# Kernel tuning notes

Hardware: AMD Instinct MI355X
Metric: run time of the kernel (lower is better)

Reference implementation:

```python
import jax, jax.numpy as jnp
import numpy as np

N_NODES = 50000
N_EDGES = 600000
D_IN, D_H1, D_H2 = 128, 128, 64


def setup_inputs() -> dict:
    key = jax.random.key(0)
    ks = jax.random.split(key, 8)
    x = jax.random.normal(ks[0], (N_NODES, D_IN), dtype=jnp.float32)
    edge_index = jax.random.randint(ks[1], (2, N_EDGES), 0, N_NODES, dtype=jnp.int64)
    # Glorot-style init for GCN weights, uniform for biases
    W1 = jax.random.normal(ks[2], (D_IN, D_H1), dtype=jnp.float32) / np.sqrt(D_IN)
    b1 = jnp.zeros((D_H1,), dtype=jnp.float32)
    W2 = jax.random.normal(ks[3], (D_H1, D_H2), dtype=jnp.float32) / np.sqrt(D_H1)
    b2 = jnp.zeros((D_H2,), dtype=jnp.float32)
    W3 = jax.random.normal(ks[4], (D_H2, 1), dtype=jnp.float32) / np.sqrt(D_H2)
    b3 = jnp.zeros((1,), dtype=jnp.float32)
    return {"x": x, "edge_index": edge_index, "W1": W1, "b1": b1,
            "W2": W2, "b2": b2, "W3": W3, "b3": b3}


def _gcn_norm(edge_index, n_nodes, dtype):
    # Add self-loops, then symmetric normalization deg^-1/2 * deg^-1/2 (PyG gcn_norm).
    loop = jnp.arange(n_nodes, dtype=edge_index.dtype)
    src = jnp.concatenate([edge_index[0], loop])
    dst = jnp.concatenate([edge_index[1], loop])
    deg = jax.ops.segment_sum(jnp.ones_like(dst, dtype=dtype), dst, num_segments=n_nodes)
    dinv = jnp.where(deg > 0, jax.lax.rsqrt(deg), 0.0)
    norm = dinv[src] * dinv[dst]  # [E+N]
    return src, dst, norm


def _gcn_conv(x, src, dst, norm, W, b, n_nodes):
    h = x @ W                       # [N, F_out]
    msg = h[src] * norm[:, None]    # gather + scale: [E+N, F_out]
    out = jax.ops.segment_sum(msg, dst, num_segments=n_nodes)  # scatter-add
    return out + b


def reference(x, edge_index, W1, b1, W2, b2, W3, b3):
    n = x.shape[0]
    src, dst, norm = _gcn_norm(edge_index, n, x.dtype)
    h = jax.nn.relu(_gcn_conv(x, src, dst, norm, W1, b1, n))
    # dropout is identity in eval mode
    h = jax.nn.relu(_gcn_conv(h, src, dst, norm, W2, b2, n))
    return h @ W3 + b3  # [N, 1]
```

## Files before the change

### kernel.cpp

```cpp
#include <hip/hip_runtime.h>

#define N_NODES 50000
#define N_EDGES 600000
#define CAP 64
#define GB1 ((N_NODES + 63) / 64)
#define FB  ((N_EDGES + 255) / 256)

typedef unsigned int u32;
typedef unsigned short u16;
typedef __attribute__((ext_vector_type(8))) short short8;
typedef __attribute__((ext_vector_type(4))) float f32x4;

__device__ __forceinline__ u16 f2bf(float f) {
    u32 u = __float_as_uint(f);
    u32 r = (u + 0x7fffu + ((u >> 16) & 1u)) >> 16;
    return (u16)r;
}
__device__ __forceinline__ float bf_lo(u32 u) { return __uint_as_float(u << 16); }
__device__ __forceinline__ float bf_hi(u32 u) { return __uint_as_float(u & 0xffff0000u); }


__global__ __launch_bounds__(256) void fill_transpose(const int* __restrict__ ei,
                                                      int* __restrict__ deg,
                                                      int* __restrict__ col,
                                                      const float* __restrict__ W1,
                                                      const float* __restrict__ W2,
                                                      u16* __restrict__ W1t,
                                                      u16* __restrict__ W2t) {
    int b = blockIdx.x, t = threadIdx.x;
    if (b < FB) {
        int e = b * 256 + t;
        if (e < N_EDGES) {
            int s = ei[e];
            int d = ei[N_EDGES + e];
            int r = atomicAdd(&deg[d], 1);
            if (r < CAP) col[((size_t)d << 6) + r] = s;
        }
    } else if (b < FB + 64) {
        int i = (b - FB) * 256 + t;
        int n = i >> 7, k = i & 127;
        W1t[i] = f2bf(W1[k * 128 + n]);
    } else {
        int j = (b - FB - 64) * 256 + t;
        int n = j >> 7, k = j & 127;
        W2t[j] = f2bf(W2[k * 64 + n]);
    }
}


#define SL 136

__global__ __launch_bounds__(256) void gemm1_k(const float* __restrict__ A,
                                               const u16* __restrict__ Bt,
                                               u16* __restrict__ out) {
    __shared__ u16 As[64 * SL];
    __shared__ u16 Bs[128 * SL];
    const int tid = threadIdx.x;
    const int m0 = blockIdx.x * 64;
    {
        int row = tid >> 2, c0 = (tid & 3) * 32;
        bool ok = (m0 + row) < N_NODES;
        const float4* src = (const float4*)&A[(size_t)(m0 + row) * 128 + c0];
        u16* dst = &As[row * SL + c0];
#pragma unroll
        for (int i = 0; i < 8; ++i) {
            float4 v = ok ? src[i] : make_float4(0.f, 0.f, 0.f, 0.f);
            u32 lo = (u32)f2bf(v.x) | ((u32)f2bf(v.y) << 16);
            u32 hi = (u32)f2bf(v.z) | ((u32)f2bf(v.w) << 16);
            *(uint2*)&dst[i * 4] = make_uint2(lo, hi);
        }
    }
    {
        int n = tid >> 1, h = (tid & 1) * 64;
        const uint4* src = (const uint4*)&Bt[n * 128 + h];
        u16* dst = &Bs[n * SL + h];
#pragma unroll
        for (int i = 0; i < 8; ++i) *(uint4*)&dst[i * 8] = src[i];
    }
    __syncthreads();

    const int l = tid & 63, w = tid >> 6;
    const int q = l >> 4, r16 = l & 15;
    const int m_off = w * 16;
    f32x4 acc[8] = {};
#pragma unroll
    for (int kt = 0; kt < 128; kt += 32) {
        short8 a = *(const short8*)&As[(m_off + r16) * SL + kt + q * 8];
        short8 bb[8];
#pragma unroll
        for (int tn = 0; tn < 8; ++tn)
            bb[tn] = *(const short8*)&Bs[(tn * 16 + r16) * SL + kt + q * 8];
#pragma unroll
        for (int tn = 0; tn < 8; ++tn)
            acc[tn] = __builtin_amdgcn_mfma_f32_16x16x32_bf16(a, bb[tn], acc[tn], 0, 0, 0);
    }
#pragma unroll
    for (int r = 0; r < 4; ++r) {
        int row = m0 + m_off + q * 4 + r;
        if (row < N_NODES) {
#pragma unroll
            for (int tn = 0; tn < 8; ++tn)
                out[(size_t)row * 128 + tn * 16 + r16] = f2bf(acc[tn][r]);
        }
    }
}


__global__ __launch_bounds__(256) void agg_gemm2(const u16* __restrict__ hs,
                                                 const int* __restrict__ deg,
                                                 const int* __restrict__ col,
                                                 const float* __restrict__ bias,
                                                 const u16* __restrict__ Bt,
                                                 u16* __restrict__ out) {
    __shared__ u16 As[64 * SL];
    __shared__ u16 Bs[64 * SL];
    const int tid = threadIdx.x;
    const int m0 = blockIdx.x * 64;
    {
        int n = tid >> 2, s0 = (tid & 3) * 32;
        const uint4* src = (const uint4*)&Bt[n * 128 + s0];
        u16* dst = &Bs[n * SL + s0];
#pragma unroll
        for (int i = 0; i < 4; ++i) *(uint4*)&dst[i * 8] = src[i];
    }
    const uint4* rows = (const uint4*)hs;
    const int lane = tid & 15;
    const int sub = lane & 7;
    const int fo = lane * 8;
#pragma unroll
    for (int p = 0; p < 4; ++p) {
        int nl = p * 16 + (tid >> 4);
        int node = m0 + nl;
        uint4 pk = make_uint4(0, 0, 0, 0);
        if (node < N_NODES) {
            int dg = deg[node];
            float dv = rsqrtf((float)(dg + 1));
            float acc[8];
            uint4 sv = rows[(size_t)node * 16 + lane];
            acc[0] = dv * bf_lo(sv.x); acc[1] = dv * bf_hi(sv.x);
            acc[2] = dv * bf_lo(sv.y); acc[3] = dv * bf_hi(sv.y);
            acc[4] = dv * bf_lo(sv.z); acc[5] = dv * bf_hi(sv.z);
            acc[6] = dv * bf_lo(sv.w); acc[7] = dv * bf_hi(sv.w);
            const int* crow = col + ((size_t)node << 6);
            int c = crow[sub];
            c = (sub < dg) ? c : 0;
            float scr = rsqrtf((float)(deg[c] + 1));
            float sc = (sub < dg) ? scr : 0.f;
            for (int r0 = 0; r0 < dg; r0 += 8) {
                int jn = r0 + 8 + sub;
                int cn = crow[jn & (CAP - 1)];
                cn = (jn < dg) ? cn : 0;
                float scnr = rsqrtf((float)(deg[cn] + 1));
                float scn = (jn < dg) ? scnr : 0.f;
#pragma unroll
                for (int jj = 0; jj < 8; ++jj) {
                    int cj = __shfl(c, jj, 16);
                    float scj = __shfl(sc, jj, 16);
                    uint4 v = rows[(size_t)cj * 16 + lane];
                    acc[0] = fmaf(scj, bf_lo(v.x), acc[0]);
                    acc[1] = fmaf(scj, bf_hi(v.x), acc[1]);
                    acc[2] = fmaf(scj, bf_lo(v.y), acc[2]);
                    acc[3] = fmaf(scj, bf_hi(v.y), acc[3]);
                    acc[4] = fmaf(scj, bf_lo(v.z), acc[4]);
                    acc[5] = fmaf(scj, bf_hi(v.z), acc[5]);
                    acc[6] = fmaf(scj, bf_lo(v.w), acc[6]);
                    acc[7] = fmaf(scj, bf_hi(v.w), acc[7]);
                }
                c = cn; sc = scn;
            }
            u32 w0[4];
#pragma unroll
            for (int jq = 0; jq < 4; ++jq) {
                u16 a = f2bf(fmaxf(fmaf(dv, acc[2 * jq], bias[fo + 2 * jq]), 0.f));
                u16 bq = f2bf(fmaxf(fmaf(dv, acc[2 * jq + 1], bias[fo + 2 * jq + 1]), 0.f));
                w0[jq] = (u32)a | ((u32)bq << 16);
            }
            pk = make_uint4(w0[0], w0[1], w0[2], w0[3]);
        }
        *(uint4*)&As[nl * SL + fo] = pk;
    }
    __syncthreads();

    const int l = tid & 63, w = tid >> 6;
    const int q = l >> 4, r16 = l & 15;
    const int m_off = w * 16;
    f32x4 acc2[4] = {};
#pragma unroll
    for (int kt = 0; kt < 128; kt += 32) {
        short8 a = *(const short8*)&As[(m_off + r16) * SL + kt + q * 8];
        short8 bb[4];
#pragma unroll
        for (int tn = 0; tn < 4; ++tn)
            bb[tn] = *(const short8*)&Bs[(tn * 16 + r16) * SL + kt + q * 8];
#pragma unroll
        for (int tn = 0; tn < 4; ++tn)
            acc2[tn] = __builtin_amdgcn_mfma_f32_16x16x32_bf16(a, bb[tn], acc2[tn], 0, 0, 0);
    }
#pragma unroll
    for (int r = 0; r < 4; ++r) {
        int row = m0 + m_off + q * 4 + r;
        if (row < N_NODES) {
            float dvr = rsqrtf((float)(deg[row] + 1));
#pragma unroll
            for (int tn = 0; tn < 4; ++tn)
                out[(size_t)row * 64 + tn * 16 + r16] = f2bf(acc2[tn][r] * dvr);
        }
    }
}


__global__ __launch_bounds__(256) void agg_final_bf(const u16* __restrict__ hs,
                                                    const int* __restrict__ deg,
                                                    const int* __restrict__ col,
                                                    const float* __restrict__ b2,
                                                    const float* __restrict__ W3,
                                                    const float* __restrict__ b3,
                                                    float* __restrict__ out) {
    int node = blockIdx.x * 32 + (threadIdx.x >> 3);
    int lane = threadIdx.x & 7;
    if (node >= N_NODES) return;
    const uint4* rows = (const uint4*)hs;
    int dg = deg[node];
    float acc[8] = {};
    auto accum = [&](uint4 v) {
        acc[0] += bf_lo(v.x); acc[1] += bf_hi(v.x);
        acc[2] += bf_lo(v.y); acc[3] += bf_hi(v.y);
        acc[4] += bf_lo(v.z); acc[5] += bf_hi(v.z);
        acc[6] += bf_lo(v.w); acc[7] += bf_hi(v.w);
    };
    accum(rows[(size_t)node * 8 + lane]);
    const int* crow = col + ((size_t)node << 6);
    int c = crow[lane];
    c = (lane < dg) ? c : 0;
    for (int r0 = 0; r0 < dg; r0 += 8) {
        int jn = r0 + 8 + lane;
        int cn = crow[jn & (CAP - 1)];
        cn = (jn < dg) ? cn : 0;
#pragma unroll
        for (int jj = 0; jj < 8; ++jj) {
            int cj = __shfl(c, jj, 8);
            uint4 v = rows[(size_t)cj * 8 + lane];
            uint4 vv = (r0 + jj < dg) ? v : make_uint4(0, 0, 0, 0);
            accum(vv);
        }
        c = cn;
    }
    float dv = rsqrtf((float)(dg + 1));
    int fo = lane * 8;
    float vsum = 0.f;
#pragma unroll
    for (int jq = 0; jq < 8; ++jq)
        vsum += fmaxf(fmaf(dv, acc[jq], b2[fo + jq]), 0.f) * W3[fo + jq];
#pragma unroll
    for (int m = 4; m > 0; m >>= 1) vsum += __shfl_xor(vsum, m, 64);
    if (lane == 0) out[node] = vsum + b3[0];
}


extern "C" void kernel_launch(void* const* d_in, const int* in_sizes, int n_in,
                              void* d_out, int out_size, void* d_ws, size_t ws_size,
                              hipStream_t stream) {
    const float* x  = (const float*)d_in[0];
    const int*   ei = (const int*)d_in[1];
    const float* W1 = (const float*)d_in[2];
    const float* b1 = (const float*)d_in[3];
    const float* W2 = (const float*)d_in[4];
    const float* b2 = (const float*)d_in[5];
    const float* W3 = (const float*)d_in[6];
    const float* b3 = (const float*)d_in[7];
    float* out = (float*)d_out;

    char* ws = (char*)d_ws;
    size_t off = 0;
    auto alloc = [&](size_t bytes) -> void* {
        void* p = ws + off;
        off = (off + bytes + 255) & ~(size_t)255;
        return p;
    };
    int* deg = (int*)alloc(N_NODES * sizeof(int));
    int* col = (int*)alloc(((size_t)N_NODES * CAP + 64) * sizeof(int));
    u16* W1t = (u16*)alloc(128 * 128 * sizeof(u16));
    u16* W2t = (u16*)alloc(64 * 128 * sizeof(u16));
    u16* hs1 = (u16*)alloc((size_t)N_NODES * 128 * sizeof(u16));
    u16* hs2 = (u16*)alloc((size_t)N_NODES * 64 * sizeof(u16));

    hipMemsetAsync(deg, 0, N_NODES * sizeof(int), stream);
    fill_transpose<<<FB + 96, 256, 0, stream>>>(ei, deg, col, W1, W2, W1t, W2t);
    gemm1_k<<<GB1, 256, 0, stream>>>(x, W1t, hs1);
    agg_gemm2<<<(N_NODES + 63) / 64, 256, 0, stream>>>(hs1, deg, col, b1, W2t, hs2);
    agg_final_bf<<<(N_NODES + 31) / 32, 256, 0, stream>>>(hs2, deg, col, b2, W3, b3, out);
}
```

Before: 168.1 us.

## Fuse all GCN stages into one persistent cooperative kernel with grid syncs

Replaces the memset and four separate kernel launches with a single cooperative persistent kernel. Grid-wide syncs separate the stages: zeroing and weight transposes, then the edge fill overlapped with gemm1, then aggregation plus gemm2, then the final aggregation. This removes launch gaps and lets the CSR fill and the first GEMM share one phase. The cost is a grid size capped by occupancy, which the largest LDS footprint (sized for gemm1) now sets for every phase, plus the expense of each grid barrier.

```diff
diff --git a/kernel.cpp b/kernel.cpp
--- a/kernel.cpp
+++ b/kernel.cpp
@@ -1,10 +1,15 @@
 #include <hip/hip_runtime.h>
+#include <hip/hip_cooperative_groups.h>
+
+namespace cg = cooperative_groups;
 
 #define N_NODES 50000
 #define N_EDGES 600000
 #define CAP 64
 #define GB1 ((N_NODES + 63) / 64)
 #define FB  ((N_EDGES + 255) / 256)
+#define AFB ((N_NODES + 31) / 32)
+#define SL 136
 
 typedef unsigned int u32;
 typedef unsigned short u16;
@@ -20,240 +25,236 @@
 __device__ __forceinline__ float bf_hi(u32 u) { return __uint_as_float(u & 0xffff0000u); }
 
 
-__global__ __launch_bounds__(256) void fill_transpose(const int* __restrict__ ei,
-                                                      int* __restrict__ deg,
-                                                      int* __restrict__ col,
-                                                      const float* __restrict__ W1,
-                                                      const float* __restrict__ W2,
-                                                      u16* __restrict__ W1t,
-                                                      u16* __restrict__ W2t) {
-    int b = blockIdx.x, t = threadIdx.x;
-    if (b < FB) {
-        int e = b * 256 + t;
-        if (e < N_EDGES) {
-            int s = ei[e];
-            int d = ei[N_EDGES + e];
-            int r = atomicAdd(&deg[d], 1);
-            if (r < CAP) col[((size_t)d << 6) + r] = s;
-        }
-    } else if (b < FB + 64) {
-        int i = (b - FB) * 256 + t;
+__global__ __launch_bounds__(256) void fused_k(
+    const float* __restrict__ x, const int* __restrict__ ei,
+    const float* __restrict__ W1, const float* __restrict__ b1,
+    const float* __restrict__ W2, const float* __restrict__ b2,
+    const float* __restrict__ W3, const float* __restrict__ b3,
+    float* __restrict__ out,
+    int* __restrict__ deg, int* __restrict__ col,
+    u16* __restrict__ W1t, u16* __restrict__ W2t,
+    u16* __restrict__ hs1, u16* __restrict__ hs2)
+{
+    __shared__ u16 As[64 * SL];
+    __shared__ u16 Bs[128 * SL];
+    cg::grid_group gg = cg::this_grid();
+    const int tid = threadIdx.x;
+    const int gsz = gridDim.x;
+    const int gtid = blockIdx.x * 256 + tid;
+    const int gstride = gsz * 256;
+
+    for (int i = gtid; i < N_NODES / 4; i += gstride)
+        ((int4*)deg)[i] = make_int4(0, 0, 0, 0);
+    for (int i = gtid; i < 128 * 128; i += gstride) {
         int n = i >> 7, k = i & 127;
         W1t[i] = f2bf(W1[k * 128 + n]);
-    } else {
-        int j = (b - FB - 64) * 256 + t;
-        int n = j >> 7, k = j & 127;
-        W2t[j] = f2bf(W2[k * 64 + n]);
-    }
-}
-
-
-#define SL 136
-
-__global__ __launch_bounds__(256) void gemm1_k(const float* __restrict__ A,
-                                               const u16* __restrict__ Bt,
-                                               u16* __restrict__ out) {
-    __shared__ u16 As[64 * SL];
-    __shared__ u16 Bs[128 * SL];
-    const int tid = threadIdx.x;
-    const int m0 = blockIdx.x * 64;
-    {
-        int row = tid >> 2, c0 = (tid & 3) * 32;
-        bool ok = (m0 + row) < N_NODES;
-        const float4* src = (const float4*)&A[(size_t)(m0 + row) * 128 + c0];
-        u16* dst = &As[row * SL + c0];
-#pragma unroll
-        for (int i = 0; i < 8; ++i) {
-            float4 v = ok ? src[i] : make_float4(0.f, 0.f, 0.f, 0.f);
-            u32 lo = (u32)f2bf(v.x) | ((u32)f2bf(v.y) << 16);
-            u32 hi = (u32)f2bf(v.z) | ((u32)f2bf(v.w) << 16);
-            *(uint2*)&dst[i * 4] = make_uint2(lo, hi);
-        }
-    }
-    {
-        int n = tid >> 1, h = (tid & 1) * 64;
-        const uint4* src = (const uint4*)&Bt[n * 128 + h];
-        u16* dst = &Bs[n * SL + h];
-#pragma unroll
-        for (int i = 0; i < 8; ++i) *(uint4*)&dst[i * 8] = src[i];
-    }
-    __syncthreads();
-
-    const int l = tid & 63, w = tid >> 6;
-    const int q = l >> 4, r16 = l & 15;
-    const int m_off = w * 16;
-    f32x4 acc[8] = {};
-#pragma unroll
-    for (int kt = 0; kt < 128; kt += 32) {
-        short8 a = *(const short8*)&As[(m_off + r16) * SL + kt + q * 8];
-        short8 bb[8];
-#pragma unroll
-        for (int tn = 0; tn < 8; ++tn)
-            bb[tn] = *(const short8*)&Bs[(tn * 16 + r16) * SL + kt + q * 8];
-#pragma unroll
-        for (int tn = 0; tn < 8; ++tn)
-            acc[tn] = __builtin_amdgcn_mfma_f32_16x16x32_bf16(a, bb[tn], acc[tn], 0, 0, 0);
-    }
-#pragma unroll
-    for (int r = 0; r < 4; ++r) {
-        int row = m0 + m_off + q * 4 + r;
-        if (row < N_NODES) {
+    }
+    for (int i = gtid; i < 64 * 128; i += gstride) {
+        int n = i >> 7, k = i & 127;
+        W2t[i] = f2bf(W2[k * 64 + n]);
+    }
+    __threadfence();
+    gg.sync();
+
+    for (int item = blockIdx.x; item < GB1 + FB; item += gsz) {
+        if (item >= GB1) {
+            int e = (item - GB1) * 256 + tid;
+            if (e < N_EDGES) {
+                int s = ei[e];
+                int d = ei[N_EDGES + e];
+                int r = atomicAdd(&deg[d], 1);
+                if (r < CAP) col[((size_t)d << 6) + r] = s;
+            }
+            continue;
+        }
+        const int m0 = item * 64;
+        __syncthreads();
+        {
+            int row = tid >> 2, c0 = (tid & 3) * 32;
+            bool ok = (m0 + row) < N_NODES;
+            const float4* src = (const float4*)&x[(size_t)(m0 + row) * 128 + c0];
+            u16* dst = &As[row * SL + c0];
+#pragma unroll
+            for (int i = 0; i < 8; ++i) {
+                float4 v = ok ? src[i] : make_float4(0.f, 0.f, 0.f, 0.f);
+                u32 lo = (u32)f2bf(v.x) | ((u32)f2bf(v.y) << 16);
+                u32 hi = (u32)f2bf(v.z) | ((u32)f2bf(v.w) << 16);
+                *(uint2*)&dst[i * 4] = make_uint2(lo, hi);
+            }
+        }
+        {
+            int n = tid >> 1, h = (tid & 1) * 64;
+            const uint4* src = (const uint4*)&W1t[n * 128 + h];
+            u16* dst = &Bs[n * SL + h];
+#pragma unroll
+            for (int i = 0; i < 8; ++i) *(uint4*)&dst[i * 8] = src[i];
+        }
+        __syncthreads();
+        const int l = tid & 63, w = tid >> 6;
+        const int q = l >> 4, r16 = l & 15;
+        const int m_off = w * 16;
+        f32x4 acc[8] = {};
+#pragma unroll
+        for (int kt = 0; kt < 128; kt += 32) {
+            short8 a = *(const short8*)&As[(m_off + r16) * SL + kt + q * 8];
+            short8 bb[8];
 #pragma unroll
             for (int tn = 0; tn < 8; ++tn)
-                out[(size_t)row * 128 + tn * 16 + r16] = f2bf(acc[tn][r]);
-        }
-    }
-}
-
-
-__global__ __launch_bounds__(256) void agg_gemm2(const u16* __restrict__ hs,
-                                                 const int* __restrict__ deg,
-                                                 const int* __restrict__ col,
-                                                 const float* __restrict__ bias,
-                                                 const u16* __restrict__ Bt,
-                                                 u16* __restrict__ out) {
-    __shared__ u16 As[64 * SL];
-    __shared__ u16 Bs[64 * SL];
-    const int tid = threadIdx.x;
-    const int m0 = blockIdx.x * 64;
-    {
-        int n = tid >> 2, s0 = (tid & 3) * 32;
-        const uint4* src = (const uint4*)&Bt[n * 128 + s0];
-        u16* dst = &Bs[n * SL + s0];
-#pragma unroll
-        for (int i = 0; i < 4; ++i) *(uint4*)&dst[i * 8] = src[i];
-    }
-    const uint4* rows = (const uint4*)hs;
-    const int lane = tid & 15;
-    const int sub = lane & 7;
-    const int fo = lane * 8;
-#pragma unroll
-    for (int p = 0; p < 4; ++p) {
-        int nl = p * 16 + (tid >> 4);
-        int node = m0 + nl;
-        uint4 pk = make_uint4(0, 0, 0, 0);
+                bb[tn] = *(const short8*)&Bs[(tn * 16 + r16) * SL + kt + q * 8];
+#pragma unroll
+            for (int tn = 0; tn < 8; ++tn)
+                acc[tn] = __builtin_amdgcn_mfma_f32_16x16x32_bf16(a, bb[tn], acc[tn], 0, 0, 0);
+        }
+#pragma unroll
+        for (int r = 0; r < 4; ++r) {
+            int row = m0 + m_off + q * 4 + r;
+            if (row < N_NODES) {
+#pragma unroll
+                for (int tn = 0; tn < 8; ++tn)
+                    hs1[(size_t)row * 128 + tn * 16 + r16] = f2bf(acc[tn][r]);
+            }
+        }
+    }
+    __threadfence();
+    gg.sync();
+
+    for (int item = blockIdx.x; item < GB1; item += gsz) {
+        const int m0 = item * 64;
+        __syncthreads();
+        {
+            int n = tid >> 2, s0 = (tid & 3) * 32;
+            const uint4* src = (const uint4*)&W2t[n * 128 + s0];
+            u16* dst = &Bs[n * SL + s0];
+#pragma unroll
+            for (int i = 0; i < 4; ++i) *(uint4*)&dst[i * 8] = src[i];
+        }
+        const uint4* rows = (const uint4*)hs1;
+        const int lane = tid & 15;
+        const int sub = lane & 7;
+        const int fo = lane * 8;
+#pragma unroll
+        for (int p = 0; p < 4; ++p) {
+            int nl = p * 16 + (tid >> 4);
+            int node = m0 + nl;
+            uint4 pk = make_uint4(0, 0, 0, 0);
+            if (node < N_NODES) {
+                int dg = deg[node];
+                float dv = rsqrtf((float)(dg + 1));
+                float acc[8];
+                uint4 sv = rows[(size_t)node * 16 + lane];
+                acc[0] = dv * bf_lo(sv.x); acc[1] = dv * bf_hi(sv.x);
+                acc[2] = dv * bf_lo(sv.y); acc[3] = dv * bf_hi(sv.y);
+                acc[4] = dv * bf_lo(sv.z); acc[5] = dv * bf_hi(sv.z);
+                acc[6] = dv * bf_lo(sv.w); acc[7] = dv * bf_hi(sv.w);
+                const int* crow = col + ((size_t)node << 6);
+                int c = crow[sub];
+                c = (sub < dg) ? c : 0;
+                float scr = rsqrtf((float)(deg[c] + 1));
+                float sc = (sub < dg) ? scr : 0.f;
+                for (int r0 = 0; r0 < dg; r0 += 8) {
+                    int jn = r0 + 8 + sub;
+                    int cn = crow[jn & (CAP - 1)];
+                    cn = (jn < dg) ? cn : 0;
+                    float scnr = rsqrtf((float)(deg[cn] + 1));
+                    float scn = (jn < dg) ? scnr : 0.f;
+#pragma unroll
+                    for (int jj = 0; jj < 8; ++jj) {
+                        int cj = __shfl(c, jj, 16);
+                        float scj = __shfl(sc, jj, 16);
+                        uint4 v = rows[(size_t)cj * 16 + lane];
+                        acc[0] = fmaf(scj, bf_lo(v.x), acc[0]);
+                        acc[1] = fmaf(scj, bf_hi(v.x), acc[1]);
+                        acc[2] = fmaf(scj, bf_lo(v.y), acc[2]);
+                        acc[3] = fmaf(scj, bf_hi(v.y), acc[3]);
+                        acc[4] = fmaf(scj, bf_lo(v.z), acc[4]);
+                        acc[5] = fmaf(scj, bf_hi(v.z), acc[5]);
+                        acc[6] = fmaf(scj, bf_lo(v.w), acc[6]);
+                        acc[7] = fmaf(scj, bf_hi(v.w), acc[7]);
+                    }
+                    c = cn; sc = scn;
+                }
+                u32 w0[4];
+#pragma unroll
+                for (int jq = 0; jq < 4; ++jq) {
+                    u16 a = f2bf(fmaxf(fmaf(dv, acc[2 * jq], b1[fo + 2 * jq]), 0.f));
+                    u16 bq = f2bf(fmaxf(fmaf(dv, acc[2 * jq + 1], b1[fo + 2 * jq + 1]), 0.f));
+                    w0[jq] = (u32)a | ((u32)bq << 16);
+                }
+                pk = make_uint4(w0[0], w0[1], w0[2], w0[3]);
+            }
+            *(uint4*)&As[nl * SL + fo] = pk;
+        }
+        __syncthreads();
+        const int l = tid & 63, w = tid >> 6;
+        const int q = l >> 4, r16 = l & 15;
+        const int m_off = w * 16;
+        f32x4 acc2[4] = {};
+#pragma unroll
+        for (int kt = 0; kt < 128; kt += 32) {
+            short8 a = *(const short8*)&As[(m_off + r16) * SL + kt + q * 8];
+            short8 bb[4];
+#pragma unroll
+            for (int tn = 0; tn < 4; ++tn)
+                bb[tn] = *(const short8*)&Bs[(tn * 16 + r16) * SL + kt + q * 8];
+#pragma unroll
+            for (int tn = 0; tn < 4; ++tn)
+                acc2[tn] = __builtin_amdgcn_mfma_f32_16x16x32_bf16(a, bb[tn], acc2[tn], 0, 0, 0);
+        }
+#pragma unroll
+        for (int r = 0; r < 4; ++r) {
+            int row = m0 + m_off + q * 4 + r;
+            if (row < N_NODES) {
+                float dvr = rsqrtf((float)(deg[row] + 1));
+#pragma unroll
+                for (int tn = 0; tn < 4; ++tn)
+                    hs2[(size_t)row * 64 + tn * 16 + r16] = f2bf(acc2[tn][r] * dvr);
+            }
+        }
+    }
+    __threadfence();
+    gg.sync();
+
+    for (int item = blockIdx.x; item < AFB; item += gsz) {
+        int node = item * 32 + (tid >> 3);
+        int lane = tid & 7;
         if (node < N_NODES) {
+            const uint4* rows = (const uint4*)hs2;
             int dg = deg[node];
-            float dv = rsqrtf((float)(dg + 1));
-            float acc[8];
-            uint4 sv = rows[(size_t)node * 16 + lane];
-            acc[0] = dv * bf_lo(sv.x); acc[1] = dv * bf_hi(sv.x);
-            acc[2] = dv * bf_lo(sv.y); acc[3] = dv * bf_hi(sv.y);
-            acc[4] = dv * bf_lo(sv.z); acc[5] = dv * bf_hi(sv.z);
-            acc[6] = dv * bf_lo(sv.w); acc[7] = dv * bf_hi(sv.w);
+            float acc[8] = {};
+            auto accum = [&](uint4 v) {
+                acc[0] += bf_lo(v.x); acc[1] += bf_hi(v.x);
+                acc[2] += bf_lo(v.y); acc[3] += bf_hi(v.y);
+                acc[4] += bf_lo(v.z); acc[5] += bf_hi(v.z);
+                acc[6] += bf_lo(v.w); acc[7] += bf_hi(v.w);
+            };
+            accum(rows[(size_t)node * 8 + lane]);
             const int* crow = col + ((size_t)node << 6);
-            int c = crow[sub];
-            c = (sub < dg) ? c : 0;
-            float scr = rsqrtf((float)(deg[c] + 1));
-            float sc = (sub < dg) ? scr : 0.f;
+            int c = crow[lane];
+            c = (lane < dg) ? c : 0;
             for (int r0 = 0; r0 < dg; r0 += 8) {
-                int jn = r0 + 8 + sub;
+                int jn = r0 + 8 + lane;
                 int cn = crow[jn & (CAP - 1)];
                 cn = (jn < dg) ? cn : 0;
-                float scnr = rsqrtf((float)(deg[cn] + 1));
-                float scn = (jn < dg) ? scnr : 0.f;
 #pragma unroll
                 for (int jj = 0; jj < 8; ++jj) {
-                    int cj = __shfl(c, jj, 16);
-                    float scj = __shfl(sc, jj, 16);
-                    uint4 v = rows[(size_t)cj * 16 + lane];
-                    acc[0] = fmaf(scj, bf_lo(v.x), acc[0]);
-                    acc[1] = fmaf(scj, bf_hi(v.x), acc[1]);
-                    acc[2] = fmaf(scj, bf_lo(v.y), acc[2]);
-                    acc[3] = fmaf(scj, bf_hi(v.y), acc[3]);
-                    acc[4] = fmaf(scj, bf_lo(v.z), acc[4]);
-                    acc[5] = fmaf(scj, bf_hi(v.z), acc[5]);
-                    acc[6] = fmaf(scj, bf_lo(v.w), acc[6]);
-                    acc[7] = fmaf(scj, bf_hi(v.w), acc[7]);
+                    int cj = __shfl(c, jj, 8);
+                    uint4 v = rows[(size_t)cj * 8 + lane];
+                    uint4 vv = (r0 + jj < dg) ? v : make_uint4(0, 0, 0, 0);
+                    accum(vv);
                 }
-                c = cn; sc = scn;
-            }
-            u32 w0[4];
-#pragma unroll
-            for (int jq = 0; jq < 4; ++jq) {
-                u16 a = f2bf(fmaxf(fmaf(dv, acc[2 * jq], bias[fo + 2 * jq]), 0.f));
-                u16 bq = f2bf(fmaxf(fmaf(dv, acc[2 * jq + 1], bias[fo + 2 * jq + 1]), 0.f));
-                w0[jq] = (u32)a | ((u32)bq << 16);
-            }
-            pk = make_uint4(w0[0], w0[1], w0[2], w0[3]);
-        }
-        *(uint4*)&As[nl * SL + fo] = pk;
-    }
-    __syncthreads();
-
-    const int l = tid & 63, w = tid >> 6;
-    const int q = l >> 4, r16 = l & 15;
-    const int m_off = w * 16;
-    f32x4 acc2[4] = {};
-#pragma unroll
-    for (int kt = 0; kt < 128; kt += 32) {
-        short8 a = *(const short8*)&As[(m_off + r16) * SL + kt + q * 8];
-        short8 bb[4];
-#pragma unroll
-        for (int tn = 0; tn < 4; ++tn)
-            bb[tn] = *(const short8*)&Bs[(tn * 16 + r16) * SL + kt + q * 8];
-#pragma unroll
-        for (int tn = 0; tn < 4; ++tn)
-            acc2[tn] = __builtin_amdgcn_mfma_f32_16x16x32_bf16(a, bb[tn], acc2[tn], 0, 0, 0);
-    }
-#pragma unroll
-    for (int r = 0; r < 4; ++r) {
-        int row = m0 + m_off + q * 4 + r;
-        if (row < N_NODES) {
-            float dvr = rsqrtf((float)(deg[row] + 1));
-#pragma unroll
-            for (int tn = 0; tn < 4; ++tn)
-                out[(size_t)row * 64 + tn * 16 + r16] = f2bf(acc2[tn][r] * dvr);
-        }
-    }
-}
-
-
-__global__ __launch_bounds__(256) void agg_final_bf(const u16* __restrict__ hs,
-                                                    const int* __restrict__ deg,
-                                                    const int* __restrict__ col,
-                                                    const float* __restrict__ b2,
-                                                    const float* __restrict__ W3,
-                                                    const float* __restrict__ b3,
-                                                    float* __restrict__ out) {
-    int node = blockIdx.x * 32 + (threadIdx.x >> 3);
-    int lane = threadIdx.x & 7;
-    if (node >= N_NODES) return;
-    const uint4* rows = (const uint4*)hs;
-    int dg = deg[node];
-    float acc[8] = {};
-    auto accum = [&](uint4 v) {
-        acc[0] += bf_lo(v.x); acc[1] += bf_hi(v.x);
-        acc[2] += bf_lo(v.y); acc[3] += bf_hi(v.y);
-        acc[4] += bf_lo(v.z); acc[5] += bf_hi(v.z);
-        acc[6] += bf_lo(v.w); acc[7] += bf_hi(v.w);
-    };
-    accum(rows[(size_t)node * 8 + lane]);
-    const int* crow = col + ((size_t)node << 6);
-    int c = crow[lane];
-    c = (lane < dg) ? c : 0;
-    for (int r0 = 0; r0 < dg; r0 += 8) {
-        int jn = r0 + 8 + lane;
-        int cn = crow[jn & (CAP - 1)];
-        cn = (jn < dg) ? cn : 0;
-#pragma unroll
-        for (int jj = 0; jj < 8; ++jj) {
-            int cj = __shfl(c, jj, 8);
-            uint4 v = rows[(size_t)cj * 8 + lane];
-            uint4 vv = (r0 + jj < dg) ? v : make_uint4(0, 0, 0, 0);
-            accum(vv);
-        }
-        c = cn;
-    }
-    float dv = rsqrtf((float)(dg + 1));
-    int fo = lane * 8;
-    float vsum = 0.f;
-#pragma unroll
-    for (int jq = 0; jq < 8; ++jq)
-        vsum += fmaxf(fmaf(dv, acc[jq], b2[fo + jq]), 0.f) * W3[fo + jq];
-#pragma unroll
-    for (int m = 4; m > 0; m >>= 1) vsum += __shfl_xor(vsum, m, 64);
-    if (lane == 0) out[node] = vsum + b3[0];
+                c = cn;
+            }
+            float dv = rsqrtf((float)(dg + 1));
+            int fo = lane * 8;
+            float vsum = 0.f;
+#pragma unroll
+            for (int jq = 0; jq < 8; ++jq)
+                vsum += fmaxf(fmaf(dv, acc[jq], b2[fo + jq]), 0.f) * W3[fo + jq];
+#pragma unroll
+            for (int m = 4; m > 0; m >>= 1) vsum += __shfl_xor(vsum, m, 64);
+            if (lane == 0) out[node] = vsum + b3[0];
+        }
+    }
 }
 
 
@@ -284,9 +285,21 @@
     u16* hs1 = (u16*)alloc((size_t)N_NODES * 128 * sizeof(u16));
     u16* hs2 = (u16*)alloc((size_t)N_NODES * 64 * sizeof(u16));
 
-    hipMemsetAsync(deg, 0, N_NODES * sizeof(int), stream);
-    fill_transpose<<<FB + 96, 256, 0, stream>>>(ei, deg, col, W1, W2, W1t, W2t);
-    gemm1_k<<<GB1, 256, 0, stream>>>(x, W1t, hs1);
-    agg_gemm2<<<(N_NODES + 63) / 64, 256, 0, stream>>>(hs1, deg, col, b1, W2t, hs2);
-    agg_final_bf<<<(N_NODES + 31) / 32, 256, 0, stream>>>(hs2, deg, col, b2, W3, b3, out);
+    static int nblk = -1;
+    if (nblk < 0) {
+        int bpc = 0;
+        if (hipOccupancyMaxActiveBlocksPerMultiprocessor(&bpc, fused_k, 256, 0) != hipSuccess
+            || bpc <= 0)
+            bpc = 1;
+        int ncu = 0;
+        if (hipDeviceGetAttribute(&ncu, hipDeviceAttributeMultiprocessorCount, 0) != hipSuccess
+            || ncu <= 0)
+            ncu = 256;
+        nblk = bpc * ncu;
+    }
+
+    void* args[] = {(void*)&x, (void*)&ei, (void*)&W1, (void*)&b1, (void*)&W2, (void*)&b2,
+                    (void*)&W3, (void*)&b3, (void*)&out, (void*)&deg, (void*)&col,
+                    (void*)&W1t, (void*)&W2t, (void*)&hs1, (void*)&hs2};
+    hipLaunchCooperativeKernel((const void*)fused_k, dim3(nblk), dim3(256), args, 0, stream);
 }
```

Result: slower. 363.9 us (+116.5%).

## Fold weight transpose and degree zeroing into GEMM kernels, drop memset

Applied to the files above, without the earlier changes.

Removes the hipMemsetAsync of the degree array and the separate weight-transpose blocks. Each GEMM block now reads the fp32 weights directly, converting and transposing them into LDS, and gemm1 also zeroes the degree array. Edge filling moves to its own kernel after gemm1, which keeps the launch count at four while dropping the memset. The cost is that every block redoes the weight conversion (W1 is 64KB per block), and gemm1 now runs before the CSR fill rather than alongside it.

```diff
diff --git a/kernel.cpp b/kernel.cpp
--- a/kernel.cpp
+++ b/kernel.cpp
@@ -5,6 +5,7 @@
 #define CAP 64
 #define GB1 ((N_NODES + 63) / 64)
 #define FB  ((N_EDGES + 255) / 256)
+#define SL 136
 
 typedef unsigned int u32;
 typedef unsigned short u16;
@@ -20,43 +21,18 @@
 __device__ __forceinline__ float bf_hi(u32 u) { return __uint_as_float(u & 0xffff0000u); }
 
 
-__global__ __launch_bounds__(256) void fill_transpose(const int* __restrict__ ei,
-                                                      int* __restrict__ deg,
-                                                      int* __restrict__ col,
-                                                      const float* __restrict__ W1,
-                                                      const float* __restrict__ W2,
-                                                      u16* __restrict__ W1t,
-                                                      u16* __restrict__ W2t) {
-    int b = blockIdx.x, t = threadIdx.x;
-    if (b < FB) {
-        int e = b * 256 + t;
-        if (e < N_EDGES) {
-            int s = ei[e];
-            int d = ei[N_EDGES + e];
-            int r = atomicAdd(&deg[d], 1);
-            if (r < CAP) col[((size_t)d << 6) + r] = s;
-        }
-    } else if (b < FB + 64) {
-        int i = (b - FB) * 256 + t;
-        int n = i >> 7, k = i & 127;
-        W1t[i] = f2bf(W1[k * 128 + n]);
-    } else {
-        int j = (b - FB - 64) * 256 + t;
-        int n = j >> 7, k = j & 127;
-        W2t[j] = f2bf(W2[k * 64 + n]);
-    }
-}
-
-
-#define SL 136
-
-__global__ __launch_bounds__(256) void gemm1_k(const float* __restrict__ A,
-                                               const u16* __restrict__ Bt,
-                                               u16* __restrict__ out) {
+__global__ __launch_bounds__(256) void gemm1z_k(const float* __restrict__ A,
+                                                const float* __restrict__ W1,
+                                                u16* __restrict__ out,
+                                                int* __restrict__ deg) {
     __shared__ u16 As[64 * SL];
     __shared__ u16 Bs[128 * SL];
     const int tid = threadIdx.x;
     const int m0 = blockIdx.x * 64;
+    {
+        int di = blockIdx.x * 256 + tid;
+        if (di < N_NODES / 4) ((int4*)deg)[di] = make_int4(0, 0, 0, 0);
+    }
     {
         int row = tid >> 2, c0 = (tid & 3) * 32;
         bool ok = (m0 + row) < N_NODES;
@@ -71,11 +47,17 @@
         }
     }
     {
-        int n = tid >> 1, h = (tid & 1) * 64;
-        const uint4* src = (const uint4*)&Bt[n * 128 + h];
-        u16* dst = &Bs[n * SL + h];
-#pragma unroll
-        for (int i = 0; i < 8; ++i) *(uint4*)&dst[i * 8] = src[i];
+        int n0 = (tid & 31) * 4, kp = tid >> 5;
+#pragma unroll
+        for (int p = 0; p < 8; ++p) {
+            int k = p * 16 + kp * 2;
+            float4 r0 = *(const float4*)&W1[(k) * 128 + n0];
+            float4 r1 = *(const float4*)&W1[(k + 1) * 128 + n0];
+            *(u32*)&Bs[(n0 + 0) * SL + k] = (u32)f2bf(r0.x) | ((u32)f2bf(r1.x) << 16);
+            *(u32*)&Bs[(n0 + 1) * SL + k] = (u32)f2bf(r0.y) | ((u32)f2bf(r1.y) << 16);
+            *(u32*)&Bs[(n0 + 2) * SL + k] = (u32)f2bf(r0.z) | ((u32)f2bf(r1.z) << 16);
+            *(u32*)&Bs[(n0 + 3) * SL + k] = (u32)f2bf(r0.w) | ((u32)f2bf(r1.w) << 16);
+        }
     }
     __syncthreads();
 
@@ -106,22 +88,41 @@
 }
 
 
+__global__ __launch_bounds__(256) void fill_k(const int* __restrict__ ei,
+                                              int* __restrict__ deg,
+                                              int* __restrict__ col) {
+    int e = blockIdx.x * 256 + threadIdx.x;
+    if (e < N_EDGES) {
+        int s = ei[e];
+        int d = ei[N_EDGES + e];
+        int r = atomicAdd(&deg[d], 1);
+        if (r < CAP) col[((size_t)d << 6) + r] = s;
+    }
+}
+
+
 __global__ __launch_bounds__(256) void agg_gemm2(const u16* __restrict__ hs,
                                                  const int* __restrict__ deg,
                                                  const int* __restrict__ col,
                                                  const float* __restrict__ bias,
-                                                 const u16* __restrict__ Bt,
+                                                 const float* __restrict__ W2,
                                                  u16* __restrict__ out) {
     __shared__ u16 As[64 * SL];
     __shared__ u16 Bs[64 * SL];
     const int tid = threadIdx.x;
     const int m0 = blockIdx.x * 64;
     {
-        int n = tid >> 2, s0 = (tid & 3) * 32;
-        const uint4* src = (const uint4*)&Bt[n * 128 + s0];
-        u16* dst = &Bs[n * SL + s0];
-#pragma unroll
-        for (int i = 0; i < 4; ++i) *(uint4*)&dst[i * 8] = src[i];
+        int n0 = (tid & 15) * 4, kp = tid >> 4;
+#pragma unroll
+        for (int p = 0; p < 4; ++p) {
+            int k = p * 32 + kp * 2;
+            float4 r0 = *(const float4*)&W2[(k) * 64 + n0];
+            float4 r1 = *(const float4*)&W2[(k + 1) * 64 + n0];
+            *(u32*)&Bs[(n0 + 0) * SL + k] = (u32)f2bf(r0.x) | ((u32)f2bf(r1.x) << 16);
+            *(u32*)&Bs[(n0 + 1) * SL + k] = (u32)f2bf(r0.y) | ((u32)f2bf(r1.y) << 16);
+            *(u32*)&Bs[(n0 + 2) * SL + k] = (u32)f2bf(r0.z) | ((u32)f2bf(r1.z) << 16);
+            *(u32*)&Bs[(n0 + 3) * SL + k] = (u32)f2bf(r0.w) | ((u32)f2bf(r1.w) << 16);
+        }
     }
     const uint4* rows = (const uint4*)hs;
     const int lane = tid & 15;
@@ -279,14 +280,11 @@
     };
     int* deg = (int*)alloc(N_NODES * sizeof(int));
     int* col = (int*)alloc(((size_t)N_NODES * CAP + 64) * sizeof(int));
-    u16* W1t = (u16*)alloc(128 * 128 * sizeof(u16));
-    u16* W2t = (u16*)alloc(64 * 128 * sizeof(u16));
     u16* hs1 = (u16*)alloc((size_t)N_NODES * 128 * sizeof(u16));
     u16* hs2 = (u16*)alloc((size_t)N_NODES * 64 * sizeof(u16));
 
-    hipMemsetAsync(deg, 0, N_NODES * sizeof(int), stream);
-    fill_transpose<<<FB + 96, 256, 0, stream>>>(ei, deg, col, W1, W2, W1t, W2t);
-    gemm1_k<<<GB1, 256, 0, stream>>>(x, W1t, hs1);
-    agg_gemm2<<<(N_NODES + 63) / 64, 256, 0, stream>>>(hs1, deg, col, b1, W2t, hs2);
+    gemm1z_k<<<GB1, 256, 0, stream>>>(x, W1, hs1, deg);
+    fill_k<<<FB, 256, 0, stream>>>(ei, deg, col);
+    agg_gemm2<<<GB1, 256, 0, stream>>>(hs1, deg, col, b1, W2, hs2);
     agg_final_bf<<<(N_NODES + 31) / 32, 256, 0, stream>>>(hs2, deg, col, b2, W3, b3, out);
 }
```

Result: slower. 173.3 us (+3.1%).

## Split layer-2 aggregation from GEMM, precompute dinv, batch neighbor gathers

Applied to the files above, without the earlier changes.

Splits the fused aggregate+GEMM2 kernel into a standalone aggregation kernel and a separate GEMM2 kernel. The aggregation kernel runs without a shared-memory footprint, requests higher occupancy via launch bounds, and issues 8 independent row loads before accumulating. Per-node deg^-1/2 is computed once into a dinv array inside gemm1, replacing repeated rsqrt-of-degree lookups. The aim is more memory-level parallelism in the gather, at the cost of an extra intermediate buffer write and read and one more kernel launch.

```diff
diff --git a/kernel.cpp b/kernel.cpp
--- a/kernel.cpp
+++ b/kernel.cpp
@@ -5,6 +5,7 @@
 #define CAP 64
 #define GB1 ((N_NODES + 63) / 64)
 #define FB  ((N_EDGES + 255) / 256)
+#define SL 136
 
 typedef unsigned int u32;
 typedef unsigned short u16;
@@ -48,15 +49,19 @@
 }
 
 
-#define SL 136
-
-__global__ __launch_bounds__(256) void gemm1_k(const float* __restrict__ A,
-                                               const u16* __restrict__ Bt,
-                                               u16* __restrict__ out) {
+__global__ __launch_bounds__(256) void gemm1d_k(const float* __restrict__ A,
+                                                const u16* __restrict__ Bt,
+                                                u16* __restrict__ out,
+                                                const int* __restrict__ deg,
+                                                float* __restrict__ dinv) {
     __shared__ u16 As[64 * SL];
     __shared__ u16 Bs[128 * SL];
     const int tid = threadIdx.x;
     const int m0 = blockIdx.x * 64;
+    {
+        int i = blockIdx.x * 256 + tid;
+        if (i < N_NODES) dinv[i] = rsqrtf((float)(deg[i] + 1));
+    }
     {
         int row = tid >> 2, c0 = (tid & 3) * 32;
         bool ok = (m0 + row) < N_NODES;
@@ -106,78 +111,100 @@
 }
 
 
-__global__ __launch_bounds__(256) void agg_gemm2(const u16* __restrict__ hs,
+__global__ __launch_bounds__(256, 8) void aggA_k(const u16* __restrict__ hs,
                                                  const int* __restrict__ deg,
+                                                 const float* __restrict__ dinv,
                                                  const int* __restrict__ col,
-                                                 const float* __restrict__ bias,
-                                                 const u16* __restrict__ Bt,
-                                                 u16* __restrict__ out) {
+                                                 const float* __restrict__ b1,
+                                                 u16* __restrict__ outb) {
+    const int lane = threadIdx.x & 15;
+    const int node = blockIdx.x * 16 + (threadIdx.x >> 4);
+    const uint4* rows = (const uint4*)hs;
+    const int dg = deg[node];
+    const float dv = dinv[node];
+    const int* crow = col + ((size_t)node << 6);
+    int c0 = crow[lane];
+    int c1 = crow[16 + lane];
+    c0 = (lane < dg) ? c0 : 0;
+    c1 = (16 + lane < dg) ? c1 : 0;
+    float s0 = (lane < dg) ? dinv[c0] : 0.f;
+    float s1 = (16 + lane < dg) ? dinv[c1] : 0.f;
+    uint4 sv = rows[(size_t)node * 16 + lane];
+
+    float acc[8];
+    acc[0] = dv * bf_lo(sv.x); acc[1] = dv * bf_hi(sv.x);
+    acc[2] = dv * bf_lo(sv.y); acc[3] = dv * bf_hi(sv.y);
+    acc[4] = dv * bf_lo(sv.z); acc[5] = dv * bf_hi(sv.z);
+    acc[6] = dv * bf_lo(sv.w); acc[7] = dv * bf_hi(sv.w);
+
+    auto batch8 = [&](int creg, float sreg, int h) {
+        uint4 v[8]; float sj[8];
+#pragma unroll
+        for (int j = 0; j < 8; ++j) {
+            int cj = __shfl(creg, h * 8 + j, 16);
+            sj[j] = __shfl(sreg, h * 8 + j, 16);
+            v[j] = rows[(size_t)cj * 16 + lane];
+        }
+#pragma unroll
+        for (int j = 0; j < 8; ++j) {
+            acc[0] = fmaf(sj[j], bf_lo(v[j].x), acc[0]);
+            acc[1] = fmaf(sj[j], bf_hi(v[j].x), acc[1]);
+            acc[2] = fmaf(sj[j], bf_lo(v[j].y), acc[2]);
+            acc[3] = fmaf(sj[j], bf_hi(v[j].y), acc[3]);
+            acc[4] = fmaf(sj[j], bf_lo(v[j].z), acc[4]);
+            acc[5] = fmaf(sj[j], bf_hi(v[j].z), acc[5]);
+            acc[6] = fmaf(sj[j], bf_lo(v[j].w), acc[6]);
+            acc[7] = fmaf(sj[j], bf_hi(v[j].w), acc[7]);
+        }
+    };
+    batch8(c0, s0, 0);
+    if (dg > 8)  batch8(c0, s0, 1);
+    if (dg > 16) batch8(c1, s1, 0);
+    if (dg > 24) batch8(c1, s1, 1);
+    for (int base = 32; base < dg; base += 16) {
+        int slot = base + lane;
+        int ct = crow[slot & (CAP - 1)];
+        ct = (slot < dg) ? ct : 0;
+        float st = (slot < dg) ? dinv[ct] : 0.f;
+        batch8(ct, st, 0);
+        if (base + 8 < dg) batch8(ct, st, 1);
+    }
+
+    const int fo = lane * 8;
+    u32 w0[4];
+#pragma unroll
+    for (int jq = 0; jq < 4; ++jq) {
+        u16 a = f2bf(fmaxf(fmaf(dv, acc[2 * jq], b1[fo + 2 * jq]), 0.f));
+        u16 b = f2bf(fmaxf(fmaf(dv, acc[2 * jq + 1], b1[fo + 2 * jq + 1]), 0.f));
+        w0[jq] = (u32)a | ((u32)b << 16);
+    }
+    *(uint4*)&outb[(size_t)node * 128 + fo] = make_uint4(w0[0], w0[1], w0[2], w0[3]);
+}
+
+
+__global__ __launch_bounds__(256) void gemm2_k(const u16* __restrict__ Ab,
+                                               const u16* __restrict__ Bt,
+                                               const float* __restrict__ dinv,
+                                               u16* __restrict__ out) {
     __shared__ u16 As[64 * SL];
     __shared__ u16 Bs[64 * SL];
     const int tid = threadIdx.x;
     const int m0 = blockIdx.x * 64;
     {
+        int row = tid >> 2, seg = (tid & 3) * 32;
+        bool ok = (m0 + row) < N_NODES;
+        const uint4* src = (const uint4*)&Ab[(size_t)(m0 + row) * 128 + seg];
+        u16* dst = &As[row * SL + seg];
+#pragma unroll
+        for (int i = 0; i < 4; ++i)
+            *(uint4*)&dst[i * 8] = ok ? src[i] : make_uint4(0, 0, 0, 0);
+    }
+    {
         int n = tid >> 2, s0 = (tid & 3) * 32;
         const uint4* src = (const uint4*)&Bt[n * 128 + s0];
         u16* dst = &Bs[n * SL + s0];
 #pragma unroll
         for (int i = 0; i < 4; ++i) *(uint4*)&dst[i * 8] = src[i];
-    }
-    const uint4* rows = (const uint4*)hs;
-    const int lane = tid & 15;
-    const int sub = lane & 7;
-    const int fo = lane * 8;
-#pragma unroll
-    for (int p = 0; p < 4; ++p) {
-        int nl = p * 16 + (tid >> 4);
-        int node = m0 + nl;
-        uint4 pk = make_uint4(0, 0, 0, 0);
-        if (node < N_NODES) {
-            int dg = deg[node];
-            float dv = rsqrtf((float)(dg + 1));
-            float acc[8];
-            uint4 sv = rows[(size_t)node * 16 + lane];
-            acc[0] = dv * bf_lo(sv.x); acc[1] = dv * bf_hi(sv.x);
-            acc[2] = dv * bf_lo(sv.y); acc[3] = dv * bf_hi(sv.y);
-            acc[4] = dv * bf_lo(sv.z); acc[5] = dv * bf_hi(sv.z);
-            acc[6] = dv * bf_lo(sv.w); acc[7] = dv * bf_hi(sv.w);
-            const int* crow = col + ((size_t)node << 6);
-            int c = crow[sub];
-            c = (sub < dg) ? c : 0;
-            float scr = rsqrtf((float)(deg[c] + 1));
-            float sc = (sub < dg) ? scr : 0.f;
-            for (int r0 = 0; r0 < dg; r0 += 8) {
-                int jn = r0 + 8 + sub;
-                int cn = crow[jn & (CAP - 1)];
-                cn = (jn < dg) ? cn : 0;
-                float scnr = rsqrtf((float)(deg[cn] + 1));
-                float scn = (jn < dg) ? scnr : 0.f;
-#pragma unroll
-                for (int jj = 0; jj < 8; ++jj) {
-                    int cj = __shfl(c, jj, 16);
-                    float scj = __shfl(sc, jj, 16);
-                    uint4 v = rows[(size_t)cj * 16 + lane];
-                    acc[0] = fmaf(scj, bf_lo(v.x), acc[0]);
-                    acc[1] = fmaf(scj, bf_hi(v.x), acc[1]);
-                    acc[2] = fmaf(scj, bf_lo(v.y), acc[2]);
-                    acc[3] = fmaf(scj, bf_hi(v.y), acc[3]);
-                    acc[4] = fmaf(scj, bf_lo(v.z), acc[4]);
-                    acc[5] = fmaf(scj, bf_hi(v.z), acc[5]);
-                    acc[6] = fmaf(scj, bf_lo(v.w), acc[6]);
-                    acc[7] = fmaf(scj, bf_hi(v.w), acc[7]);
-                }
-                c = cn; sc = scn;
-            }
-            u32 w0[4];
-#pragma unroll
-            for (int jq = 0; jq < 4; ++jq) {
-                u16 a = f2bf(fmaxf(fmaf(dv, acc[2 * jq], bias[fo + 2 * jq]), 0.f));
-                u16 bq = f2bf(fmaxf(fmaf(dv, acc[2 * jq + 1], bias[fo + 2 * jq + 1]), 0.f));
-                w0[jq] = (u32)a | ((u32)bq << 16);
-            }
-            pk = make_uint4(w0[0], w0[1], w0[2], w0[3]);
-        }
-        *(uint4*)&As[nl * SL + fo] = pk;
     }
     __syncthreads();
 
@@ -200,7 +227,7 @@
     for (int r = 0; r < 4; ++r) {
         int row = m0 + m_off + q * 4 + r;
         if (row < N_NODES) {
-            float dvr = rsqrtf((float)(deg[row] + 1));
+            float dvr = dinv[row];
 #pragma unroll
             for (int tn = 0; tn < 4; ++tn)
                 out[(size_t)row * 64 + tn * 16 + r16] = f2bf(acc2[tn][r] * dvr);
@@ -277,16 +304,19 @@
         off = (off + bytes + 255) & ~(size_t)255;
         return p;
     };
-    int* deg = (int*)alloc(N_NODES * sizeof(int));
-    int* col = (int*)alloc(((size_t)N_NODES * CAP + 64) * sizeof(int));
-    u16* W1t = (u16*)alloc(128 * 128 * sizeof(u16));
-    u16* W2t = (u16*)alloc(64 * 128 * sizeof(u16));
-    u16* hs1 = (u16*)alloc((size_t)N_NODES * 128 * sizeof(u16));
-    u16* hs2 = (u16*)alloc((size_t)N_NODES * 64 * sizeof(u16));
+    int*   deg  = (int*)alloc(N_NODES * sizeof(int));
+    int*   col  = (int*)alloc(((size_t)N_NODES * CAP + 64) * sizeof(int));
+    float* dinv = (float*)alloc(N_NODES * sizeof(float));
+    u16*   W1t  = (u16*)alloc(128 * 128 * sizeof(u16));
+    u16*   W2t  = (u16*)alloc(64 * 128 * sizeof(u16));
+    u16*   hs1  = (u16*)alloc((size_t)N_NODES * 128 * sizeof(u16));
+    u16*   hs1b = (u16*)alloc((size_t)N_NODES * 128 * sizeof(u16));
+    u16*   hs2  = (u16*)alloc((size_t)N_NODES * 64 * sizeof(u16));
 
     hipMemsetAsync(deg, 0, N_NODES * sizeof(int), stream);
     fill_transpose<<<FB + 96, 256, 0, stream>>>(ei, deg, col, W1, W2, W1t, W2t);
-    gemm1_k<<<GB1, 256, 0, stream>>>(x, W1t, hs1);
-    agg_gemm2<<<(N_NODES + 63) / 64, 256, 0, stream>>>(hs1, deg, col, b1, W2t, hs2);
+    gemm1d_k<<<GB1, 256, 0, stream>>>(x, W1t, hs1, deg, dinv);
+    aggA_k<<<N_NODES / 16, 256, 0, stream>>>(hs1, deg, dinv, col, b1, hs1b);
+    gemm2_k<<<GB1, 256, 0, stream>>>(hs1b, W2t, dinv, hs2);
     agg_final_bf<<<(N_NODES + 31) / 32, 256, 0, stream>>>(hs2, deg, col, b2, W3, b3, out);
 }
```

New measurement: 217.8 us. +29.5%, slower.
